# Performance work log

Measured on AMD Instinct MI355X. Metric: run time of the kernel, lower is better.

The kernel has to match this reference:

```python
import jax, jax.numpy as jnp
import numpy as np

H, T, D = 16, 2048, 1024
DH = D // H  # 64


def setup_inputs() -> dict:
    key = jax.random.key(0)
    ks = jax.random.split(key, 6)
    state = jax.random.normal(ks[0], (H, DH, DH), jnp.float32) * 0.02  # per-head recurrent state
    x = jax.random.normal(ks[1], (T, D), jnp.float32)
    done = jax.random.uniform(ks[2], (T,)) < (4.0 / T)  # sparse episode-reset flags (bool)
    w_qkv = jax.random.normal(ks[3], (D, 3 * D), jnp.float32) / np.sqrt(D)
    b_qkv = jnp.zeros((3 * D,), jnp.float32)
    w_out = jax.random.normal(ks[4], (D, D), jnp.float32) / np.sqrt(D)
    b_out = jnp.zeros((D,), jnp.float32)
    return {"state": state, "x": x, "done": done, "w_qkv": w_qkv,
            "b_qkv": b_qkv, "w_out": w_out, "b_out": b_out}


def _mha_forward(state, x, done, w_qkv, b_qkv, w_out, b_out):
    # qkv projection; einops 'T (QKV H Dh) -> QKV H T Dh'
    qkv = (x @ w_qkv + b_qkv).reshape(T, 3, H, DH).transpose(1, 2, 0, 3)
    q, k, v = qkv[0], qkv[1], qkv[2]  # each (H, T, Dh)

    cum = jnp.cumsum(done.astype(jnp.int32))  # inclusive cumsum, as in done.cumsum()
    before_first = cum == 0            # tokens before first reset (attend to carried state)
    after_last = cum == cum[-1]        # tokens after last reset (feed new state)
    done_any = cum[-1] > 0

    # make_attn_mask(done): causal AND no reset index i with s < i <= t.
    # The scanned mask equals: causal & (cum[t] == cum[s]) (same-segment).
    t_idx = jnp.arange(T)
    mask = (t_idx[:, None] >= t_idx[None, :]) & (cum[:, None] == cum[None, :])  # (T, T)

    attn = jnp.where(mask[None], jnp.einsum('htd,hsd->hts', q, k), 0.0)  # mask * (q @ k.T)
    q_bef = q * before_first[None, :, None]
    out = jnp.einsum('hts,hsd->htd', attn, v) + jnp.einsum('htd,hde->hte', q_bef, state)

    k_aft = k * after_last[None, :, None]
    v_aft = v * after_last[None, :, None]
    s_new = jnp.einsum('htd,hte->hde', k_aft, v_aft)  # k_aft.T @ v_aft per head
    new_state = jnp.where(done_any, s_new, state + s_new)

    # 'H T Dh -> T (H Dh)' then output projection
    x_out = out.transpose(1, 0, 2).reshape(T, D) @ w_out + b_out
    return new_state, x_out


def reference(state, x, done, w_qkv, b_qkv, w_out, b_out):
    return _mha_forward(state, x, done, w_qkv, b_qkv, w_out, b_out)
```

## Files before the change

### kernel.cpp

```cpp
#include <hip/hip_runtime.h>

#define TT 2048
#define DD 1024
#define HH 16
#define DH 64
#define QKV_N 3072
#define QKW 2048

typedef __attribute__((ext_vector_type(8))) short bf16x8;
typedef __attribute__((ext_vector_type(4))) short short4v;
typedef __attribute__((ext_vector_type(4))) float f32x4;

__device__ inline short f2bf(float f) {
    union { float f; unsigned u; } v; v.f = f;
    unsigned r = v.u + 0x7fff + ((v.u >> 16) & 1);
    return (short)(r >> 16);
}

__device__ inline f32x4 mfma16(bf16x8 a, bf16x8 b, f32x4 c) {
    return __builtin_amdgcn_mfma_f32_16x16x32_bf16(a, b, c, 0, 0, 0);
}

__device__ __forceinline__ void gload16(const void* g, void* l) {
    __builtin_amdgcn_global_load_lds(
        (const __attribute__((address_space(1))) unsigned int*)g,
        (__attribute__((address_space(3))) unsigned int*)l, 16, 0, 0);
}

__device__ void transpose_tile(const float* __restrict__ in, short* __restrict__ out,
                               int R, int C, int r0, int c0, float (*tile)[65]) {
    int tid = threadIdx.x;
#pragma unroll
    for (int p = 0; p < 4; ++p) {
        int ch = tid + p * 256;
        int r = ch >> 4, c4 = (ch & 15) * 4;
        float4 v = *(const float4*)&in[(size_t)(r0 + r) * C + c0 + c4];
        tile[r][c4] = v.x; tile[r][c4 + 1] = v.y; tile[r][c4 + 2] = v.z; tile[r][c4 + 3] = v.w;
    }
    __syncthreads();
#pragma unroll
    for (int p = 0; p < 2; ++p) {
        int ch = tid + p * 256;
        int c = ch >> 3, r8 = (ch & 7) * 8;
        short tmp[8];
#pragma unroll
        for (int i = 0; i < 8; ++i) tmp[i] = f2bf(tile[r8 + i][c]);
        *(float4*)&out[(size_t)(c0 + c) * R + r0 + r8] = *(float4*)tmp;
    }
}

__global__ __launch_bounds__(256) void prep_kernel(const float* __restrict__ x,
                                                   const float* __restrict__ w_qkv,
                                                   const float* __restrict__ w_out,
                                                   const float* __restrict__ state,
                                                   const int* __restrict__ done,
                                                   short* __restrict__ x_bf,
                                                   short* __restrict__ wqT,
                                                   short* __restrict__ woT,
                                                   short* __restrict__ stT,
                                                   float* __restrict__ stout,
                                                   int* __restrict__ seg,
                                                   int* __restrict__ totalp,
                                                   int* __restrict__ aux) {
    __shared__ float tile[64][65];
    __shared__ int scanbuf[2048 + 512 + 1];
    int b = blockIdx.x;
    int tid = threadIdx.x;
    if (b < 1024) {
        int i = (b * 256 + tid) * 8;
        float4 a = *(const float4*)&x[i];
        float4 c = *(const float4*)&x[i + 4];
        short tmp[8] = {f2bf(a.x), f2bf(a.y), f2bf(a.z), f2bf(a.w),
                        f2bf(c.x), f2bf(c.y), f2bf(c.z), f2bf(c.w)};
        *(float4*)&x_bf[i] = *(float4*)tmp;
    } else if (b < 1792) {
        int bb = b - 1024;
        transpose_tile(w_qkv, wqT, DD, QKV_N, (bb & 15) * 64, (bb >> 4) * 64, tile);
    } else if (b < 2048) {
        int bb = b - 1792;
        transpose_tile(w_out, woT, DD, DD, (bb & 15) * 64, (bb >> 4) * 64, tile);
    } else if (b < 2064) {
        int h = b - 2048;
        transpose_tile(state + (size_t)h * 4096, stT + (size_t)h * 4096, DH, DH, 0, 0, tile);
    } else if (b < 2128) {
        __shared__ int anyf;
        if (tid == 0) anyf = 0;
        __syncthreads();
        int acc = 0;
#pragma unroll
        for (int i = 0; i < 8; ++i) acc |= done[tid * 8 + i];
        if (acc) anyf = 1;
        __syncthreads();
        int f = ((b - 2064) * 256 + tid) * 4;
        float4 v = anyf ? make_float4(0.f, 0.f, 0.f, 0.f) : *(const float4*)&state[f];
        *(float4*)&stout[f] = v;
    } else {
        int* segl = scanbuf;
        int* part = scanbuf + 2048;
        int* excl = scanbuf + 2304;
        int base = tid * 8;
        int local[8];
        int run = 0;
#pragma unroll
        for (int i = 0; i < 8; ++i) { run += (done[base + i] != 0) ? 1 : 0; local[i] = run; }
        part[tid] = run;
        __syncthreads();
        if (tid < 64) {
            int p4[4];
#pragma unroll
            for (int i = 0; i < 4; ++i) p4[i] = part[tid * 4 + i];
            int s = p4[0] + p4[1] + p4[2] + p4[3];
            int v = s;
#pragma unroll
            for (int off = 1; off < 64; off <<= 1) {
                int u = __shfl_up(v, off);
                if (tid >= off) v += u;
            }
            int ex = v - s;
#pragma unroll
            for (int i = 0; i < 4; ++i) { excl[tid * 4 + i] = ex; ex += p4[i]; }
            if (tid == 63) { totalp[0] = v; scanbuf[2560] = v; }
        }
        __syncthreads();
        int off = excl[tid];
#pragma unroll
        for (int i = 0; i < 8; ++i) {
            int sv = off + local[i];
            seg[base + i] = sv;
            segl[base + i] = sv;
        }
        __syncthreads();
        if (tid < 33) {
            int target = (tid < 32) ? segl[tid * 64] : scanbuf[2560];
            int lo = 0, hi = 2047;
            while (lo < hi) { int mid = (lo + hi) >> 1; if (segl[mid] >= target) hi = mid; else lo = mid + 1; }
            aux[tid] = lo >> 6;
        }
    }
}

__global__ __launch_bounds__(256, 3) void gemm_qkv(const short* __restrict__ A,
                                                   const short* __restrict__ BT,
                                                   const float* __restrict__ bias,
                                                   short* __restrict__ qk,
                                                   short* __restrict__ vt) {
    __shared__ __align__(16) short As[2][2][64 * 32];
    __shared__ __align__(16) short Bs[2][2][128 * 32];
    const int K = DD;
    int tid = threadIdx.x;
    int wave = tid >> 6, lane = tid & 63;
    int quad = lane >> 4, l15 = lane & 15;
    int m0 = blockIdx.x * 64, n0 = blockIdx.y * 128;
    int wr = (wave >> 1) * 32, wc = (wave & 1) * 64;

    int srow = wave * 16 + (lane >> 2);
    int scol = (lane & 3) * 8;
    const short* Ag = A + (size_t)(m0 + srow) * K + scol;
    const short* Bg = BT + (size_t)(n0 + srow) * K + scol;

#pragma unroll
    for (int ks = 0; ks < 2; ++ks) {
        gload16(Ag + ks * 32, &As[0][ks][(wave * 16) * 32]);
        gload16(Bg + ks * 32, &Bs[0][ks][(wave * 16) * 32]);
        gload16(Bg + (size_t)64 * K + ks * 32, &Bs[0][ks][(64 + wave * 16) * 32]);
    }
    __syncthreads();

    f32x4 acc[2][4] = {};
    int cur = 0;
    for (int k0 = 0; k0 < K; k0 += 64, cur ^= 1) {
        if (k0 + 64 < K) {
#pragma unroll
            for (int ks = 0; ks < 2; ++ks) {
                gload16(Ag + k0 + 64 + ks * 32, &As[cur ^ 1][ks][(wave * 16) * 32]);
                gload16(Bg + k0 + 64 + ks * 32, &Bs[cur ^ 1][ks][(wave * 16) * 32]);
                gload16(Bg + (size_t)64 * K + k0 + 64 + ks * 32,
                        &Bs[cur ^ 1][ks][(64 + wave * 16) * 32]);
            }
        }
#pragma unroll
        for (int ks = 0; ks < 2; ++ks) {
            bf16x8 af[2], bfr[4];
#pragma unroll
            for (int i = 0; i < 2; ++i)
                af[i]  = *(const bf16x8*)&As[cur][ks][(wr + i * 16 + l15) * 32 + quad * 8];
#pragma unroll
            for (int j = 0; j < 4; ++j)
                bfr[j] = *(const bf16x8*)&Bs[cur][ks][(wc + j * 16 + l15) * 32 + quad * 8];
#pragma unroll
            for (int i = 0; i < 2; ++i)
#pragma unroll
                for (int j = 0; j < 4; ++j)
                    acc[i][j] = mfma16(af[i], bfr[j], acc[i][j]);
        }
        __syncthreads();
    }

    if (n0 < 2048) {
#pragma unroll
        for (int i = 0; i < 2; ++i)
#pragma unroll
            for (int j = 0; j < 4; ++j)
#pragma unroll
                for (int r = 0; r < 4; ++r) {
                    int row = m0 + wr + i * 16 + quad * 4 + r;
                    int col = n0 + wc + j * 16 + l15;
                    qk[(size_t)row * QKW + col] = f2bf(acc[i][j][r] + bias[col]);
                }
    } else {
#pragma unroll
        for (int j = 0; j < 4; ++j) {
            int col = n0 + wc + j * 16 + l15;
            float bv = bias[col];
            int eg = col - 2048;
            int hh = eg >> 6, e = eg & 63;
#pragma unroll
            for (int i = 0; i < 2; ++i) {
                int tb = m0 + wr + i * 16 + quad * 4;
                short4v pk;
#pragma unroll
                for (int r = 0; r < 4; ++r) pk[r] = f2bf(acc[i][j][r] + bv);
                *(short4v*)&vt[(size_t)hh * (DH * TT) + (size_t)e * TT + tb] = pk;
            }
        }
    }
}

__global__ __launch_bounds__(256) void attn_mfma(const short* __restrict__ qk,
                                                 const short* __restrict__ vt,
                                                 const short* __restrict__ stT,
                                                 const int* __restrict__ seg,
                                                 const int* __restrict__ totalp,
                                                 const int* __restrict__ aux,
                                                 short* __restrict__ outb,
                                                 float* __restrict__ nsout) {
    __shared__ __align__(16) short Qh[2][64 * 32];
    __shared__ __align__(16) short Kh[2][2][64 * 32];
    __shared__ __align__(16) short Vh[2][2][64 * 32];
    __shared__ __align__(16) short Ss[64 * 72];

    int h = blockIdx.x, tt = blockIdx.y, z = blockIdx.z;
    int t0 = tt * 64;
    int tid = threadIdx.x, wave = tid >> 6, lane = tid & 63;
    int quad = lane >> 4, l15 = lane & 15;
    int myt = wave * 16;
    const short* vbase = vt + (size_t)h * (DH * TT);

    if (z == 1) {
        if (tt < aux[32]) return;
        int total = totalp[0];
        int myd = wave * 16;
        short* K0 = Kh[0][0];
        short* K1 = Kh[0][1];
        bool keep = (seg[t0 + lane] == total);
        const short* src = qk + (size_t)(t0 + lane) * QKW + 1024 + h * DH + myd;
        union { float4 f; short s[8]; } u0, u1;
        u0.f = keep ? *(const float4*)src : make_float4(0.f, 0.f, 0.f, 0.f);
        u1.f = keep ? *(const float4*)(src + 8) : make_float4(0.f, 0.f, 0.f, 0.f);
        short* dst = (lane < 32) ? &K0[lane] : &K1[lane - 32];
#pragma unroll
        for (int i = 0; i < 8; ++i) {
            dst[(myd + i) * 32] = u0.s[i];
            dst[(myd + 8 + i) * 32] = u1.s[i];
        }
        bf16x8 a0 = *(const bf16x8*)&K0[(myd + l15) * 32 + quad * 8];
        bf16x8 a1 = *(const bf16x8*)&K1[(myd + l15) * 32 + quad * 8];
        f32x4 acc2[4] = {};
#pragma unroll
        for (int j = 0; j < 4; ++j) {
            const short* vrow = vbase + (size_t)(j * 16 + l15) * TT + t0 + quad * 8;
            bf16x8 b0 = *(const bf16x8*)vrow;
            bf16x8 b1 = *(const bf16x8*)(vrow + 32);
            acc2[j] = mfma16(a0, b0, acc2[j]);
            acc2[j] = mfma16(a1, b1, acc2[j]);
        }
        float* oh = nsout + (size_t)h * 4096;
#pragma unroll
        for (int j = 0; j < 4; ++j)
#pragma unroll
            for (int r = 0; r < 4; ++r)
                atomicAdd(&oh[(myd + quad * 4 + r) * DH + j * 16 + l15], acc2[j][r]);
        return;
    }

    int st0 = aux[tt];
    int sr = lane >> 2;
    int ch = lane & 3;
    const short* kg = qk + 1024 + h * DH;

    {
#pragma unroll
        for (int h2 = 0; h2 < 2; ++h2)
            gload16(qk + (size_t)(t0 + myt + sr) * QKW + h * DH + h2 * 32 + ch * 8,
                    &Qh[h2][myt * 32]);
        int s0 = st0 * 64;
        gload16(kg + (size_t)(s0 + myt + sr) * QKW + ch * 8,      &Kh[0][0][myt * 32]);
        gload16(kg + (size_t)(s0 + myt + sr) * QKW + 32 + ch * 8, &Kh[0][1][myt * 32]);
        gload16(vbase + (size_t)(myt + sr) * TT + s0 + ch * 8,    &Vh[0][0][myt * 32]);
        gload16(vbase + (size_t)(myt + sr) * TT + s0 + 32 + ch * 8, &Vh[0][1][myt * 32]);
    }
    __syncthreads();

    bf16x8 af[2];
#pragma unroll
    for (int h2 = 0; h2 < 2; ++h2)
        af[h2] = *(const bf16x8*)&Qh[h2][(myt + l15) * 32 + quad * 8];

    int t_val = t0 + myt + l15;
    int seg_lane = seg[t_val];

    f32x4 acc2[4] = {};
    if (seg[t0] == 0) {
        const short* sb = stT + (size_t)h * 4096;
#pragma unroll
        for (int j = 0; j < 4; ++j)
#pragma unroll
            for (int h2 = 0; h2 < 2; ++h2) {
                bf16x8 a = *(const bf16x8*)(sb + (j * 16 + l15) * 64 + h2 * 32 + quad * 8);
                acc2[j] = mfma16(a, af[h2], acc2[j]);
            }
        if (seg_lane != 0) {
#pragma unroll
            for (int j = 0; j < 4; ++j)
#pragma unroll
                for (int r = 0; r < 4; ++r) acc2[j][r] = 0.f;
        }
    }

    int p = 0;
    for (int st = st0; st <= tt; ++st, p ^= 1) {
        if (st != st0) __syncthreads();
        if (st + 1 <= tt) {
            int s1 = (st + 1) * 64;
            gload16(kg + (size_t)(s1 + myt + sr) * QKW + ch * 8,        &Kh[p ^ 1][0][myt * 32]);
            gload16(kg + (size_t)(s1 + myt + sr) * QKW + 32 + ch * 8,   &Kh[p ^ 1][1][myt * 32]);
            gload16(vbase + (size_t)(myt + sr) * TT + s1 + ch * 8,      &Vh[p ^ 1][0][myt * 32]);
            gload16(vbase + (size_t)(myt + sr) * TT + s1 + 32 + ch * 8, &Vh[p ^ 1][1][myt * 32]);
        }
        int s0 = st * 64;

        f32x4 sacc[4] = {};
#pragma unroll
        for (int j = 0; j < 4; ++j)
#pragma unroll
            for (int h2 = 0; h2 < 2; ++h2) {
                bf16x8 kb = *(const bf16x8*)&Kh[p][h2][(j * 16 + l15) * 32 + quad * 8];
                sacc[j] = mfma16(kb, af[h2], sacc[j]);
            }
        int4 seg4[4];
#pragma unroll
        for (int j = 0; j < 4; ++j)
            seg4[j] = *(const int4*)&seg[s0 + j * 16 + quad * 4];
#pragma unroll
        for (int j = 0; j < 4; ++j) {
            short4v pk;
#pragma unroll
            for (int r = 0; r < 4; ++r) {
                int s_val = s0 + j * 16 + quad * 4 + r;
                int sv = (r == 0) ? seg4[j].x : (r == 1) ? seg4[j].y : (r == 2) ? seg4[j].z : seg4[j].w;
                bool ok = (sv == seg_lane) && (s_val <= t_val);
                pk[r] = ok ? f2bf(sacc[j][r]) : (short)0;
            }
            *(short4v*)&Ss[(myt + l15) * 72 + j * 16 + quad * 4] = pk;
        }
        bf16x8 sf[2];
#pragma unroll
        for (int h2 = 0; h2 < 2; ++h2)
            sf[h2] = *(const bf16x8*)&Ss[(myt + l15) * 72 + h2 * 32 + quad * 8];
#pragma unroll
        for (int j = 0; j < 4; ++j)
#pragma unroll
            for (int h2 = 0; h2 < 2; ++h2) {
                bf16x8 vb = *(const bf16x8*)&Vh[p][h2][(j * 16 + l15) * 32 + quad * 8];
                acc2[j] = mfma16(vb, sf[h2], acc2[j]);
            }
    }

#pragma unroll
    for (int j = 0; j < 4; ++j) {
        short4v pk;
#pragma unroll
        for (int r = 0; r < 4; ++r) pk[r] = f2bf(acc2[j][r]);
        *(short4v*)&outb[(size_t)t_val * DD + h * DH + j * 16 + quad * 4] = pk;
    }
}

__global__ __launch_bounds__(256) void gemm_out(const short* __restrict__ A,
                                                const short* __restrict__ BT,
                                                const float* __restrict__ bias,
                                                float* __restrict__ x_out) {
    __shared__ __align__(16) short As[2][2][64 * 32];
    __shared__ __align__(16) short Bs[2][2][128 * 32];
    const int K = DD, N = DD;
    int tid = threadIdx.x;
    int wave = tid >> 6, lane = tid & 63;
    int quad = lane >> 4, l15 = lane & 15;
    int m0 = blockIdx.x * 64, n0 = blockIdx.y * 128;
    int wr = (wave >> 1) * 32, wc = (wave & 1) * 64;

    int srow = wave * 16 + (lane >> 2);
    int scol = (lane & 3) * 8;
    const short* Ag = A + (size_t)(m0 + srow) * K + scol;
    const short* Bg = BT + (size_t)(n0 + srow) * K + scol;

#pragma unroll
    for (int ks = 0; ks < 2; ++ks) {
        gload16(Ag + ks * 32, &As[0][ks][(wave * 16) * 32]);
        gload16(Bg + ks * 32, &Bs[0][ks][(wave * 16) * 32]);
        gload16(Bg + (size_t)64 * K + ks * 32, &Bs[0][ks][(64 + wave * 16) * 32]);
    }
    __syncthreads();

    f32x4 acc[2][4] = {};
    int cur = 0;
    for (int k0 = 0; k0 < K; k0 += 64, cur ^= 1) {
        if (k0 + 64 < K) {
#pragma unroll
            for (int ks = 0; ks < 2; ++ks) {
                gload16(Ag + k0 + 64 + ks * 32, &As[cur ^ 1][ks][(wave * 16) * 32]);
                gload16(Bg + k0 + 64 + ks * 32, &Bs[cur ^ 1][ks][(wave * 16) * 32]);
                gload16(Bg + (size_t)64 * K + k0 + 64 + ks * 32,
                        &Bs[cur ^ 1][ks][(64 + wave * 16) * 32]);
            }
        }
#pragma unroll
        for (int ks = 0; ks < 2; ++ks) {
            bf16x8 af[2], bfr[4];
#pragma unroll
            for (int i = 0; i < 2; ++i)
                af[i]  = *(const bf16x8*)&As[cur][ks][(wr + i * 16 + l15) * 32 + quad * 8];
#pragma unroll
            for (int j = 0; j < 4; ++j)
                bfr[j] = *(const bf16x8*)&Bs[cur][ks][(wc + j * 16 + l15) * 32 + quad * 8];
#pragma unroll
            for (int i = 0; i < 2; ++i)
#pragma unroll
                for (int j = 0; j < 4; ++j)
                    acc[i][j] = mfma16(af[i], bfr[j], acc[i][j]);
        }
        __syncthreads();
    }

#pragma unroll
    for (int i = 0; i < 2; ++i)
#pragma unroll
        for (int j = 0; j < 4; ++j) {
            int col = n0 + wc + j * 16 + l15;
            float bv = bias[col];
#pragma unroll
            for (int r = 0; r < 4; ++r) {
                int row = m0 + wr + i * 16 + quad * 4 + r;
                x_out[(size_t)row * N + col] = acc[i][j][r] + bv;
            }
        }
}

extern "C" void kernel_launch(void* const* d_in, const int* in_sizes, int n_in,
                              void* d_out, int out_size, void* d_ws, size_t ws_size,
                              hipStream_t stream) {
    const float* state = (const float*)d_in[0];
    const float* x     = (const float*)d_in[1];
    const int*   done  = (const int*)d_in[2];
    const float* w_qkv = (const float*)d_in[3];
    const float* b_qkv = (const float*)d_in[4];
    const float* w_out = (const float*)d_in[5];
    const float* b_out = (const float*)d_in[6];

    char* ws = (char*)d_ws;
    int*   seg    = (int*)ws;
    int*   totalp = (int*)(ws + 8192);
    int*   aux    = (int*)(ws + 8256);
    short* wqT    = (short*)(ws + 8448);
    short* woT    = (short*)(ws + 6299904);
    short* stT    = (short*)(ws + 8397056);
    short* qk     = (short*)(ws + 8528128);
    short* vt     = (short*)(ws + 16916736);
    short* xbf_outb = (short*)(ws + 21111040);

    float* new_state_out = (float*)d_out;
    float* x_out         = (float*)d_out + HH * DH * DH;

    prep_kernel<<<2129, 256, 0, stream>>>(x, w_qkv, w_out, state, done,
                                          xbf_outb, wqT, woT, stT,
                                          new_state_out, seg, totalp, aux);

    gemm_qkv<<<dim3(TT / 64, QKV_N / 128), 256, 0, stream>>>(
        xbf_outb, wqT, b_qkv, qk, vt);

    attn_mfma<<<dim3(HH, TT / 64, 2), 256, 0, stream>>>(
        qk, vt, stT, seg, totalp, aux, xbf_outb, new_state_out);

    gemm_out<<<dim3(TT / 64, DD / 128), 256, 0, stream>>>(
        xbf_outb, woT, b_out, x_out);
}
```

Measured before the change: 147.2 us.

## Fuse prep into GEMMs: convert fp32 inputs in-loop, drop transposes and state atomics

Removes the separate prep kernel. The QKV and output GEMMs now load fp32 x and the weights straight from global memory through registers, convert them to bf16 and store into LDS with a register-staged double buffer, so no pre-transposed bf16 weight copies are built. The scan and state-transpose blocks move into extra blocks of the QKV GEMM launch. The new-state computation becomes one block per head that loops over the tail chunks and writes the result directly, replacing the zeroing pass and atomicAdds. In exchange, B loads are strided scalar fp32 reads and each GEMM tile converts its operands on the fly.

Measured after the change: 157.9 us. 1.07x slower.

```diff
diff --git a/kernel.cpp b/kernel.cpp
--- a/kernel.cpp
+++ b/kernel.cpp
@@ -49,152 +49,151 @@
     }
 }
 
-__global__ __launch_bounds__(256) void prep_kernel(const float* __restrict__ x,
+__global__ __launch_bounds__(256, 3) void gemm_qkv(const float* __restrict__ x,
                                                    const float* __restrict__ w_qkv,
-                                                   const float* __restrict__ w_out,
                                                    const float* __restrict__ state,
                                                    const int* __restrict__ done,
-                                                   short* __restrict__ x_bf,
-                                                   short* __restrict__ wqT,
-                                                   short* __restrict__ woT,
+                                                   const float* __restrict__ bias,
+                                                   short* __restrict__ qk,
+                                                   short* __restrict__ vt,
                                                    short* __restrict__ stT,
-                                                   float* __restrict__ stout,
                                                    int* __restrict__ seg,
                                                    int* __restrict__ totalp,
                                                    int* __restrict__ aux) {
-    __shared__ float tile[64][65];
-    __shared__ int scanbuf[2048 + 512 + 1];
+    union Sh {
+        struct { short As[2][2][64 * 32]; short Bs[2][2][128 * 32]; } g;
+        struct { float tile[64][65]; int scanbuf[2561]; } p;
+    };
+    __shared__ __align__(16) Sh sh;
     int b = blockIdx.x;
     int tid = threadIdx.x;
-    if (b < 1024) {
-        int i = (b * 256 + tid) * 8;
-        float4 a = *(const float4*)&x[i];
-        float4 c = *(const float4*)&x[i + 4];
-        short tmp[8] = {f2bf(a.x), f2bf(a.y), f2bf(a.z), f2bf(a.w),
-                        f2bf(c.x), f2bf(c.y), f2bf(c.z), f2bf(c.w)};
-        *(float4*)&x_bf[i] = *(float4*)tmp;
-    } else if (b < 1792) {
-        int bb = b - 1024;
-        transpose_tile(w_qkv, wqT, DD, QKV_N, (bb & 15) * 64, (bb >> 4) * 64, tile);
-    } else if (b < 2048) {
-        int bb = b - 1792;
-        transpose_tile(w_out, woT, DD, DD, (bb & 15) * 64, (bb >> 4) * 64, tile);
-    } else if (b < 2064) {
-        int h = b - 2048;
-        transpose_tile(state + (size_t)h * 4096, stT + (size_t)h * 4096, DH, DH, 0, 0, tile);
-    } else if (b < 2128) {
-        __shared__ int anyf;
-        if (tid == 0) anyf = 0;
-        __syncthreads();
-        int acc = 0;
-#pragma unroll
-        for (int i = 0; i < 8; ++i) acc |= done[tid * 8 + i];
-        if (acc) anyf = 1;
-        __syncthreads();
-        int f = ((b - 2064) * 256 + tid) * 4;
-        float4 v = anyf ? make_float4(0.f, 0.f, 0.f, 0.f) : *(const float4*)&state[f];
-        *(float4*)&stout[f] = v;
-    } else {
-        int* segl = scanbuf;
-        int* part = scanbuf + 2048;
-        int* excl = scanbuf + 2304;
-        int base = tid * 8;
-        int local[8];
-        int run = 0;
-#pragma unroll
-        for (int i = 0; i < 8; ++i) { run += (done[base + i] != 0) ? 1 : 0; local[i] = run; }
-        part[tid] = run;
-        __syncthreads();
-        if (tid < 64) {
-            int p4[4];
-#pragma unroll
-            for (int i = 0; i < 4; ++i) p4[i] = part[tid * 4 + i];
-            int s = p4[0] + p4[1] + p4[2] + p4[3];
-            int v = s;
-#pragma unroll
-            for (int off = 1; off < 64; off <<= 1) {
-                int u = __shfl_up(v, off);
-                if (tid >= off) v += u;
-            }
-            int ex = v - s;
-#pragma unroll
-            for (int i = 0; i < 4; ++i) { excl[tid * 4 + i] = ex; ex += p4[i]; }
-            if (tid == 63) { totalp[0] = v; scanbuf[2560] = v; }
-        }
-        __syncthreads();
-        int off = excl[tid];
-#pragma unroll
-        for (int i = 0; i < 8; ++i) {
-            int sv = off + local[i];
-            seg[base + i] = sv;
-            segl[base + i] = sv;
-        }
-        __syncthreads();
-        if (tid < 33) {
-            int target = (tid < 32) ? segl[tid * 64] : scanbuf[2560];
-            int lo = 0, hi = 2047;
-            while (lo < hi) { int mid = (lo + hi) >> 1; if (segl[mid] >= target) hi = mid; else lo = mid + 1; }
-            aux[tid] = lo >> 6;
-        }
-    }
-}
-
-__global__ __launch_bounds__(256, 3) void gemm_qkv(const short* __restrict__ A,
-                                                   const short* __restrict__ BT,
-                                                   const float* __restrict__ bias,
-                                                   short* __restrict__ qk,
-                                                   short* __restrict__ vt) {
-    __shared__ __align__(16) short As[2][2][64 * 32];
-    __shared__ __align__(16) short Bs[2][2][128 * 32];
-    const int K = DD;
-    int tid = threadIdx.x;
+
+    if (b >= 768) {
+        if (b < 784) {
+            int h = b - 768;
+            transpose_tile(state + (size_t)h * 4096, stT + (size_t)h * 4096,
+                           DH, DH, 0, 0, sh.p.tile);
+        } else {
+            int* segl = sh.p.scanbuf;
+            int* part = sh.p.scanbuf + 2048;
+            int* excl = sh.p.scanbuf + 2304;
+            int base = tid * 8;
+            int local[8];
+            int run = 0;
+#pragma unroll
+            for (int i = 0; i < 8; ++i) { run += (done[base + i] != 0) ? 1 : 0; local[i] = run; }
+            part[tid] = run;
+            __syncthreads();
+            if (tid < 64) {
+                int p4[4];
+#pragma unroll
+                for (int i = 0; i < 4; ++i) p4[i] = part[tid * 4 + i];
+                int s = p4[0] + p4[1] + p4[2] + p4[3];
+                int v = s;
+#pragma unroll
+                for (int off = 1; off < 64; off <<= 1) {
+                    int u = __shfl_up(v, off);
+                    if (tid >= off) v += u;
+                }
+                int ex = v - s;
+#pragma unroll
+                for (int i = 0; i < 4; ++i) { excl[tid * 4 + i] = ex; ex += p4[i]; }
+                if (tid == 63) { totalp[0] = v; sh.p.scanbuf[2560] = v; }
+            }
+            __syncthreads();
+            int off = excl[tid];
+#pragma unroll
+            for (int i = 0; i < 8; ++i) {
+                int sv = off + local[i];
+                seg[base + i] = sv;
+                segl[base + i] = sv;
+            }
+            __syncthreads();
+            if (tid < 33) {
+                int target = (tid < 32) ? segl[tid * 64] : sh.p.scanbuf[2560];
+                int lo = 0, hi = 2047;
+                while (lo < hi) { int mid = (lo + hi) >> 1; if (segl[mid] >= target) hi = mid; else lo = mid + 1; }
+                aux[tid] = lo >> 6;
+            }
+        }
+        return;
+    }
+
+    const int K = DD, NT = 16;
     int wave = tid >> 6, lane = tid & 63;
     int quad = lane >> 4, l15 = lane & 15;
-    int m0 = blockIdx.x * 64, n0 = blockIdx.y * 128;
+    int m0 = (b & 31) * 64, n0 = (b >> 5) * 128;
     int wr = (wave >> 1) * 32, wc = (wave & 1) * 64;
 
-    int srow = wave * 16 + (lane >> 2);
-    int scol = (lane & 3) * 8;
-    const short* Ag = A + (size_t)(m0 + srow) * K + scol;
-    const short* Bg = BT + (size_t)(n0 + srow) * K + scol;
-
-#pragma unroll
-    for (int ks = 0; ks < 2; ++ks) {
-        gload16(Ag + ks * 32, &As[0][ks][(wave * 16) * 32]);
-        gload16(Bg + ks * 32, &Bs[0][ks][(wave * 16) * 32]);
-        gload16(Bg + (size_t)64 * K + ks * 32, &Bs[0][ks][(64 + wave * 16) * 32]);
-    }
+    int arow = tid >> 2, kc = tid & 3;
+    const float* Abase = x + (size_t)(m0 + arow) * K + kc * 8;
+    int bn = tid & 127, kh = tid >> 7;
+    const float* Bbase = w_qkv + (size_t)(kh * 16) * QKV_N + n0 + bn;
+
+    float4 areg[2][2];
+    float  breg[2][16];
+
+#define LOADR(t)                                                              \
+    {                                                                         \
+        _Pragma("unroll")                                                     \
+        for (int ks = 0; ks < 2; ++ks) {                                      \
+            const float* ap = Abase + (t) * 64 + ks * 32;                     \
+            areg[ks][0] = *(const float4*)ap;                                 \
+            areg[ks][1] = *(const float4*)(ap + 4);                           \
+            const float* bp = Bbase + (size_t)((t) * 64 + ks * 32) * QKV_N;   \
+            _Pragma("unroll")                                                 \
+            for (int i = 0; i < 16; ++i)                                      \
+                breg[ks][i] = bp[(size_t)i * QKV_N];                          \
+        }                                                                     \
+    }
+
+#define WRITER(buf)                                                           \
+    {                                                                         \
+        _Pragma("unroll")                                                     \
+        for (int ks = 0; ks < 2; ++ks) {                                      \
+            short ta[8] = {f2bf(areg[ks][0].x), f2bf(areg[ks][0].y),          \
+                           f2bf(areg[ks][0].z), f2bf(areg[ks][0].w),          \
+                           f2bf(areg[ks][1].x), f2bf(areg[ks][1].y),          \
+                           f2bf(areg[ks][1].z), f2bf(areg[ks][1].w)};         \
+            *(float4*)&sh.g.As[buf][ks][arow * 32 + kc * 8] = *(float4*)ta;   \
+            short tb[16];                                                     \
+            _Pragma("unroll")                                                 \
+            for (int i = 0; i < 16; ++i) tb[i] = f2bf(breg[ks][i]);           \
+            *(float4*)&sh.g.Bs[buf][ks][bn * 32 + kh * 16]     = ((float4*)tb)[0]; \
+            *(float4*)&sh.g.Bs[buf][ks][bn * 32 + kh * 16 + 8] = ((float4*)tb)[1]; \
+        }                                                                     \
+    }
+
+    LOADR(0);
+    WRITER(0);
+    LOADR(1);
     __syncthreads();
 
     f32x4 acc[2][4] = {};
-    int cur = 0;
-    for (int k0 = 0; k0 < K; k0 += 64, cur ^= 1) {
-        if (k0 + 64 < K) {
-#pragma unroll
-            for (int ks = 0; ks < 2; ++ks) {
-                gload16(Ag + k0 + 64 + ks * 32, &As[cur ^ 1][ks][(wave * 16) * 32]);
-                gload16(Bg + k0 + 64 + ks * 32, &Bs[cur ^ 1][ks][(wave * 16) * 32]);
-                gload16(Bg + (size_t)64 * K + k0 + 64 + ks * 32,
-                        &Bs[cur ^ 1][ks][(64 + wave * 16) * 32]);
-            }
-        }
+#pragma unroll 1
+    for (int t = 0; t < NT; ++t) {
+        int cur = t & 1;
 #pragma unroll
         for (int ks = 0; ks < 2; ++ks) {
             bf16x8 af[2], bfr[4];
 #pragma unroll
             for (int i = 0; i < 2; ++i)
-                af[i]  = *(const bf16x8*)&As[cur][ks][(wr + i * 16 + l15) * 32 + quad * 8];
+                af[i]  = *(const bf16x8*)&sh.g.As[cur][ks][(wr + i * 16 + l15) * 32 + quad * 8];
 #pragma unroll
             for (int j = 0; j < 4; ++j)
-                bfr[j] = *(const bf16x8*)&Bs[cur][ks][(wc + j * 16 + l15) * 32 + quad * 8];
+                bfr[j] = *(const bf16x8*)&sh.g.Bs[cur][ks][(wc + j * 16 + l15) * 32 + quad * 8];
 #pragma unroll
             for (int i = 0; i < 2; ++i)
 #pragma unroll
                 for (int j = 0; j < 4; ++j)
                     acc[i][j] = mfma16(af[i], bfr[j], acc[i][j]);
         }
+        if (t + 1 < NT) WRITER(cur ^ 1);
+        if (t + 2 < NT) LOADR(t + 2);
         __syncthreads();
     }
+#undef LOADR
+#undef WRITER
 
     if (n0 < 2048) {
 #pragma unroll
@@ -229,6 +228,7 @@
 __global__ __launch_bounds__(256) void attn_mfma(const short* __restrict__ qk,
                                                  const short* __restrict__ vt,
                                                  const short* __restrict__ stT,
+                                                 const float* __restrict__ state,
                                                  const int* __restrict__ seg,
                                                  const int* __restrict__ totalp,
                                                  const int* __restrict__ aux,
@@ -239,50 +239,57 @@
     __shared__ __align__(16) short Vh[2][2][64 * 32];
     __shared__ __align__(16) short Ss[64 * 72];
 
-    int h = blockIdx.x, tt = blockIdx.y, z = blockIdx.z;
-    int t0 = tt * 64;
+    int h = blockIdx.x, tt = blockIdx.y;
     int tid = threadIdx.x, wave = tid >> 6, lane = tid & 63;
     int quad = lane >> 4, l15 = lane & 15;
     int myt = wave * 16;
     const short* vbase = vt + (size_t)h * (DH * TT);
 
-    if (z == 1) {
-        if (tt < aux[32]) return;
+    if (tt == 32) {
         int total = totalp[0];
+        int ct0 = aux[32];
         int myd = wave * 16;
         short* K0 = Kh[0][0];
         short* K1 = Kh[0][1];
-        bool keep = (seg[t0 + lane] == total);
-        const short* src = qk + (size_t)(t0 + lane) * QKW + 1024 + h * DH + myd;
-        union { float4 f; short s[8]; } u0, u1;
-        u0.f = keep ? *(const float4*)src : make_float4(0.f, 0.f, 0.f, 0.f);
-        u1.f = keep ? *(const float4*)(src + 8) : make_float4(0.f, 0.f, 0.f, 0.f);
-        short* dst = (lane < 32) ? &K0[lane] : &K1[lane - 32];
-#pragma unroll
-        for (int i = 0; i < 8; ++i) {
-            dst[(myd + i) * 32] = u0.s[i];
-            dst[(myd + 8 + i) * 32] = u1.s[i];
-        }
-        bf16x8 a0 = *(const bf16x8*)&K0[(myd + l15) * 32 + quad * 8];
-        bf16x8 a1 = *(const bf16x8*)&K1[(myd + l15) * 32 + quad * 8];
         f32x4 acc2[4] = {};
-#pragma unroll
-        for (int j = 0; j < 4; ++j) {
-            const short* vrow = vbase + (size_t)(j * 16 + l15) * TT + t0 + quad * 8;
-            bf16x8 b0 = *(const bf16x8*)vrow;
-            bf16x8 b1 = *(const bf16x8*)(vrow + 32);
-            acc2[j] = mfma16(a0, b0, acc2[j]);
-            acc2[j] = mfma16(a1, b1, acc2[j]);
-        }
+        for (int ct = ct0; ct < 32; ++ct) {
+            int t0c = ct * 64;
+            bool keep = (seg[t0c + lane] == total);
+            const short* src = qk + (size_t)(t0c + lane) * QKW + 1024 + h * DH + myd;
+            union { float4 f; short s[8]; } u0, u1;
+            u0.f = keep ? *(const float4*)src : make_float4(0.f, 0.f, 0.f, 0.f);
+            u1.f = keep ? *(const float4*)(src + 8) : make_float4(0.f, 0.f, 0.f, 0.f);
+            short* dst = (lane < 32) ? &K0[lane] : &K1[lane - 32];
+#pragma unroll
+            for (int i = 0; i < 8; ++i) {
+                dst[(myd + i) * 32] = u0.s[i];
+                dst[(myd + 8 + i) * 32] = u1.s[i];
+            }
+            bf16x8 a0 = *(const bf16x8*)&K0[(myd + l15) * 32 + quad * 8];
+            bf16x8 a1 = *(const bf16x8*)&K1[(myd + l15) * 32 + quad * 8];
+#pragma unroll
+            for (int j = 0; j < 4; ++j) {
+                const short* vrow = vbase + (size_t)(j * 16 + l15) * TT + t0c + quad * 8;
+                bf16x8 b0 = *(const bf16x8*)vrow;
+                bf16x8 b1 = *(const bf16x8*)(vrow + 32);
+                acc2[j] = mfma16(a0, b0, acc2[j]);
+                acc2[j] = mfma16(a1, b1, acc2[j]);
+            }
+        }
+        bool carry = (total == 0);
         float* oh = nsout + (size_t)h * 4096;
+        const float* sh0 = state + (size_t)h * 4096;
 #pragma unroll
         for (int j = 0; j < 4; ++j)
 #pragma unroll
-            for (int r = 0; r < 4; ++r)
-                atomicAdd(&oh[(myd + quad * 4 + r) * DH + j * 16 + l15], acc2[j][r]);
+            for (int r = 0; r < 4; ++r) {
+                int idx = (myd + quad * 4 + r) * DH + j * 16 + l15;
+                oh[idx] = acc2[j][r] + (carry ? sh0[idx] : 0.f);
+            }
         return;
     }
 
+    int t0 = tt * 64;
     int st0 = aux[tt];
     int sr = lane >> 2;
     int ch = lane & 3;
@@ -385,13 +392,13 @@
     }
 }
 
-__global__ __launch_bounds__(256) void gemm_out(const short* __restrict__ A,
-                                                const short* __restrict__ BT,
-                                                const float* __restrict__ bias,
-                                                float* __restrict__ x_out) {
+__global__ __launch_bounds__(256, 3) void gemm_out(const short* __restrict__ A,
+                                                   const float* __restrict__ w_out,
+                                                   const float* __restrict__ bias,
+                                                   float* __restrict__ x_out) {
     __shared__ __align__(16) short As[2][2][64 * 32];
     __shared__ __align__(16) short Bs[2][2][128 * 32];
-    const int K = DD, N = DD;
+    const int K = DD, N = DD, NT = 16;
     int tid = threadIdx.x;
     int wave = tid >> 6, lane = tid & 63;
     int quad = lane >> 4, l15 = lane & 15;
@@ -401,28 +408,49 @@
     int srow = wave * 16 + (lane >> 2);
     int scol = (lane & 3) * 8;
     const short* Ag = A + (size_t)(m0 + srow) * K + scol;
-    const short* Bg = BT + (size_t)(n0 + srow) * K + scol;
-
-#pragma unroll
-    for (int ks = 0; ks < 2; ++ks) {
-        gload16(Ag + ks * 32, &As[0][ks][(wave * 16) * 32]);
-        gload16(Bg + ks * 32, &Bs[0][ks][(wave * 16) * 32]);
-        gload16(Bg + (size_t)64 * K + ks * 32, &Bs[0][ks][(64 + wave * 16) * 32]);
-    }
+
+    int bn = tid & 127, kh = tid >> 7;
+    const float* Bbase = w_out + (size_t)(kh * 16) * N + n0 + bn;
+    float breg[2][16];
+
+#define LOADB(t)                                                              \
+    {                                                                         \
+        _Pragma("unroll")                                                     \
+        for (int ks = 0; ks < 2; ++ks) {                                      \
+            const float* bp = Bbase + (size_t)((t) * 64 + ks * 32) * N;       \
+            _Pragma("unroll")                                                 \
+            for (int i = 0; i < 16; ++i) breg[ks][i] = bp[(size_t)i * N];     \
+        }                                                                     \
+    }
+#define WRITEB(buf)                                                           \
+    {                                                                         \
+        _Pragma("unroll")                                                     \
+        for (int ks = 0; ks < 2; ++ks) {                                      \
+            short tb[16];                                                     \
+            _Pragma("unroll")                                                 \
+            for (int i = 0; i < 16; ++i) tb[i] = f2bf(breg[ks][i]);           \
+            *(float4*)&Bs[buf][ks][bn * 32 + kh * 16]     = ((float4*)tb)[0]; \
+            *(float4*)&Bs[buf][ks][bn * 32 + kh * 16 + 8] = ((float4*)tb)[1]; \
+        }                                                                     \
+    }
+#define LOADA(t, buf)                                                         \
+    {                                                                         \
+        _Pragma("unroll")                                                     \
+        for (int ks = 0; ks < 2; ++ks)                                        \
+            gload16(Ag + (t) * 64 + ks * 32, &As[buf][ks][(wave * 16) * 32]); \
+    }
+
+    LOADB(0);
+    WRITEB(0);
+    LOADB(1);
+    LOADA(0, 0);
     __syncthreads();
 
     f32x4 acc[2][4] = {};
-    int cur = 0;
-    for (int k0 = 0; k0 < K; k0 += 64, cur ^= 1) {
-        if (k0 + 64 < K) {
-#pragma unroll
-            for (int ks = 0; ks < 2; ++ks) {
-                gload16(Ag + k0 + 64 + ks * 32, &As[cur ^ 1][ks][(wave * 16) * 32]);
-                gload16(Bg + k0 + 64 + ks * 32, &Bs[cur ^ 1][ks][(wave * 16) * 32]);
-                gload16(Bg + (size_t)64 * K + k0 + 64 + ks * 32,
-                        &Bs[cur ^ 1][ks][(64 + wave * 16) * 32]);
-            }
-        }
+#pragma unroll 1
+    for (int t = 0; t < NT; ++t) {
+        int cur = t & 1;
+        if (t + 1 < NT) LOADA(t + 1, cur ^ 1);
 #pragma unroll
         for (int ks = 0; ks < 2; ++ks) {
             bf16x8 af[2], bfr[4];
@@ -438,8 +466,13 @@
                 for (int j = 0; j < 4; ++j)
                     acc[i][j] = mfma16(af[i], bfr[j], acc[i][j]);
         }
+        if (t + 1 < NT) WRITEB(cur ^ 1);
+        if (t + 2 < NT) LOADB(t + 2);
         __syncthreads();
     }
+#undef LOADB
+#undef WRITEB
+#undef LOADA
 
 #pragma unroll
     for (int i = 0; i < 2; ++i)
@@ -470,26 +503,20 @@
     int*   seg    = (int*)ws;
     int*   totalp = (int*)(ws + 8192);
     int*   aux    = (int*)(ws + 8256);
-    short* wqT    = (short*)(ws + 8448);
-    short* woT    = (short*)(ws + 6299904);
-    short* stT    = (short*)(ws + 8397056);
-    short* qk     = (short*)(ws + 8528128);
-    short* vt     = (short*)(ws + 16916736);
-    short* xbf_outb = (short*)(ws + 21111040);
+    short* stT    = (short*)(ws + 8448);
+    short* qk     = (short*)(ws + 139520);
+    short* vt     = (short*)(ws + 8528128);
+    short* outb   = (short*)(ws + 12722432);
 
     float* new_state_out = (float*)d_out;
     float* x_out         = (float*)d_out + HH * DH * DH;
 
-    prep_kernel<<<2129, 256, 0, stream>>>(x, w_qkv, w_out, state, done,
-                                          xbf_outb, wqT, woT, stT,
-                                          new_state_out, seg, totalp, aux);
-
-    gemm_qkv<<<dim3(TT / 64, QKV_N / 128), 256, 0, stream>>>(
-        xbf_outb, wqT, b_qkv, qk, vt);
-
-    attn_mfma<<<dim3(HH, TT / 64, 2), 256, 0, stream>>>(
-        qk, vt, stT, seg, totalp, aux, xbf_outb, new_state_out);
+    gemm_qkv<<<785, 256, 0, stream>>>(x, w_qkv, state, done, b_qkv,
+                                      qk, vt, stT, seg, totalp, aux);
+
+    attn_mfma<<<dim3(HH, 33), 256, 0, stream>>>(
+        qk, vt, stT, state, seg, totalp, aux, outb, new_state_out);
 
     gemm_out<<<dim3(TT / 64, DD / 128), 256, 0, stream>>>(
-        xbf_outb, woT, b_out, x_out);
-}
+        outb, w_out, b_out, x_out);
+}
```

## Remap grids to XCD-aware 1D order and fold state update into per-head blocks

Applied to the files above, without the earlier changes.

The GEMM and attention launches become flat 1D grids, with block IDs remapped so that consecutive tiles land on the same XCD (blockIdx & 7), which should improve L2 locality on the multi-die GPU. The new-state computation moves from many per-tile blocks doing atomicAdd into one block per head that loops over the tail tiles and writes the result directly, adding the carried state when no reset occurred. This removes the prep-kernel state copy and the atomics. In exchange each head's state update now runs serially over tiles inside a single block.

Measured after the change: 149.2 us. Within noise of the previous version (+1.3%).

```diff
diff --git a/kernel.cpp b/kernel.cpp
--- a/kernel.cpp
+++ b/kernel.cpp
@@ -58,7 +58,6 @@
                                                    short* __restrict__ wqT,
                                                    short* __restrict__ woT,
                                                    short* __restrict__ stT,
-                                                   float* __restrict__ stout,
                                                    int* __restrict__ seg,
                                                    int* __restrict__ totalp,
                                                    int* __restrict__ aux) {
@@ -82,18 +81,6 @@
     } else if (b < 2064) {
         int h = b - 2048;
         transpose_tile(state + (size_t)h * 4096, stT + (size_t)h * 4096, DH, DH, 0, 0, tile);
-    } else if (b < 2128) {
-        __shared__ int anyf;
-        if (tid == 0) anyf = 0;
-        __syncthreads();
-        int acc = 0;
-#pragma unroll
-        for (int i = 0; i < 8; ++i) acc |= done[tid * 8 + i];
-        if (acc) anyf = 1;
-        __syncthreads();
-        int f = ((b - 2064) * 256 + tid) * 4;
-        float4 v = anyf ? make_float4(0.f, 0.f, 0.f, 0.f) : *(const float4*)&state[f];
-        *(float4*)&stout[f] = v;
     } else {
         int* segl = scanbuf;
         int* part = scanbuf + 2048;
@@ -150,7 +137,8 @@
     int tid = threadIdx.x;
     int wave = tid >> 6, lane = tid & 63;
     int quad = lane >> 4, l15 = lane & 15;
-    int m0 = blockIdx.x * 64, n0 = blockIdx.y * 128;
+    int vid = (blockIdx.x & 7) * 96 + (blockIdx.x >> 3);
+    int m0 = (vid & 31) * 64, n0 = (vid >> 5) * 128;
     int wr = (wave >> 1) * 32, wc = (wave & 1) * 64;
 
     int srow = wave * 16 + (lane >> 2);
@@ -229,6 +217,7 @@
 __global__ __launch_bounds__(256) void attn_mfma(const short* __restrict__ qk,
                                                  const short* __restrict__ vt,
                                                  const short* __restrict__ stT,
+                                                 const float* __restrict__ state,
                                                  const int* __restrict__ seg,
                                                  const int* __restrict__ totalp,
                                                  const int* __restrict__ aux,
@@ -239,50 +228,60 @@
     __shared__ __align__(16) short Vh[2][2][64 * 32];
     __shared__ __align__(16) short Ss[64 * 72];
 
-    int h = blockIdx.x, tt = blockIdx.y, z = blockIdx.z;
-    int t0 = tt * 64;
+    int vid = (blockIdx.x & 7) * 66 + (blockIdx.x >> 3);
+    int h = vid / 33, tt = vid % 33;
     int tid = threadIdx.x, wave = tid >> 6, lane = tid & 63;
     int quad = lane >> 4, l15 = lane & 15;
     int myt = wave * 16;
     const short* vbase = vt + (size_t)h * (DH * TT);
 
-    if (z == 1) {
-        if (tt < aux[32]) return;
+    if (tt == 32) {
         int total = totalp[0];
+        int ct0 = aux[32];
         int myd = wave * 16;
         short* K0 = Kh[0][0];
         short* K1 = Kh[0][1];
-        bool keep = (seg[t0 + lane] == total);
-        const short* src = qk + (size_t)(t0 + lane) * QKW + 1024 + h * DH + myd;
-        union { float4 f; short s[8]; } u0, u1;
-        u0.f = keep ? *(const float4*)src : make_float4(0.f, 0.f, 0.f, 0.f);
-        u1.f = keep ? *(const float4*)(src + 8) : make_float4(0.f, 0.f, 0.f, 0.f);
-        short* dst = (lane < 32) ? &K0[lane] : &K1[lane - 32];
-#pragma unroll
-        for (int i = 0; i < 8; ++i) {
-            dst[(myd + i) * 32] = u0.s[i];
-            dst[(myd + 8 + i) * 32] = u1.s[i];
-        }
-        bf16x8 a0 = *(const bf16x8*)&K0[(myd + l15) * 32 + quad * 8];
-        bf16x8 a1 = *(const bf16x8*)&K1[(myd + l15) * 32 + quad * 8];
         f32x4 acc2[4] = {};
-#pragma unroll
-        for (int j = 0; j < 4; ++j) {
-            const short* vrow = vbase + (size_t)(j * 16 + l15) * TT + t0 + quad * 8;
-            bf16x8 b0 = *(const bf16x8*)vrow;
-            bf16x8 b1 = *(const bf16x8*)(vrow + 32);
-            acc2[j] = mfma16(a0, b0, acc2[j]);
-            acc2[j] = mfma16(a1, b1, acc2[j]);
-        }
+        for (int ct = ct0; ct < 32; ++ct) {
+            int t0c = ct * 64;
+            bool keep = (seg[t0c + lane] == total);
+            const short* src = qk + (size_t)(t0c + lane) * QKW + 1024 + h * DH + myd;
+            union { float4 f; short s[8]; } u0, u1;
+            u0.f = keep ? *(const float4*)src : make_float4(0.f, 0.f, 0.f, 0.f);
+            u1.f = keep ? *(const float4*)(src + 8) : make_float4(0.f, 0.f, 0.f, 0.f);
+            short* dst = (lane < 32) ? &K0[lane] : &K1[lane - 32];
+#pragma unroll
+            for (int i = 0; i < 8; ++i) {
+                dst[(myd + i) * 32] = u0.s[i];
+                dst[(myd + 8 + i) * 32] = u1.s[i];
+            }
+            __syncthreads();
+            bf16x8 a0 = *(const bf16x8*)&K0[(myd + l15) * 32 + quad * 8];
+            bf16x8 a1 = *(const bf16x8*)&K1[(myd + l15) * 32 + quad * 8];
+#pragma unroll
+            for (int j = 0; j < 4; ++j) {
+                const short* vrow = vbase + (size_t)(j * 16 + l15) * TT + t0c + quad * 8;
+                bf16x8 b0 = *(const bf16x8*)vrow;
+                bf16x8 b1 = *(const bf16x8*)(vrow + 32);
+                acc2[j] = mfma16(a0, b0, acc2[j]);
+                acc2[j] = mfma16(a1, b1, acc2[j]);
+            }
+            __syncthreads();
+        }
+        bool carry = (totalp[0] == 0);
         float* oh = nsout + (size_t)h * 4096;
+        const float* sh0 = state + (size_t)h * 4096;
 #pragma unroll
         for (int j = 0; j < 4; ++j)
 #pragma unroll
-            for (int r = 0; r < 4; ++r)
-                atomicAdd(&oh[(myd + quad * 4 + r) * DH + j * 16 + l15], acc2[j][r]);
+            for (int r = 0; r < 4; ++r) {
+                int idx = (myd + quad * 4 + r) * DH + j * 16 + l15;
+                oh[idx] = acc2[j][r] + (carry ? sh0[idx] : 0.f);
+            }
         return;
     }
 
+    int t0 = tt * 64;
     int st0 = aux[tt];
     int sr = lane >> 2;
     int ch = lane & 3;
@@ -395,7 +394,8 @@
     int tid = threadIdx.x;
     int wave = tid >> 6, lane = tid & 63;
     int quad = lane >> 4, l15 = lane & 15;
-    int m0 = blockIdx.x * 64, n0 = blockIdx.y * 128;
+    int vid = (blockIdx.x & 7) * 32 + (blockIdx.x >> 3);
+    int m0 = (vid & 31) * 64, n0 = (vid >> 5) * 128;
     int wr = (wave >> 1) * 32, wc = (wave & 1) * 64;
 
     int srow = wave * 16 + (lane >> 2);
@@ -480,16 +480,14 @@
     float* new_state_out = (float*)d_out;
     float* x_out         = (float*)d_out + HH * DH * DH;
 
-    prep_kernel<<<2129, 256, 0, stream>>>(x, w_qkv, w_out, state, done,
+    prep_kernel<<<2065, 256, 0, stream>>>(x, w_qkv, w_out, state, done,
                                           xbf_outb, wqT, woT, stT,
-                                          new_state_out, seg, totalp, aux);
-
-    gemm_qkv<<<dim3(TT / 64, QKV_N / 128), 256, 0, stream>>>(
-        xbf_outb, wqT, b_qkv, qk, vt);
-
-    attn_mfma<<<dim3(HH, TT / 64, 2), 256, 0, stream>>>(
-        qk, vt, stT, seg, totalp, aux, xbf_outb, new_state_out);
-
-    gemm_out<<<dim3(TT / 64, DD / 128), 256, 0, stream>>>(
-        xbf_outb, woT, b_out, x_out);
-}
+                                          seg, totalp, aux);
+
+    gemm_qkv<<<768, 256, 0, stream>>>(xbf_outb, wqT, b_qkv, qk, vt);
+
+    attn_mfma<<<528, 256, 0, stream>>>(
+        qk, vt, stT, state, seg, totalp, aux, xbf_outb, new_state_out);
+
+    gemm_out<<<256, 256, 0, stream>>>(xbf_outb, woT, b_out, x_out);
+}
```
